# Performance work log

Measured on AMD Instinct MI355X. Metric: run time of the kernel, lower is better.

Reference implementation:

```python
import jax, jax.numpy as jnp
import numpy as np

EPS = 1e-6
K = 16
TEMP = 1.0
RES_SCALE = 0.5
CLAMP_MAX = 50.0


def _knn_indices(x, k):
    # x: (B,N,3) -> idx (B,N,k), self excluded; squared dist preserves ordering
    sq = jnp.sum(x * x, axis=-1)                      # (B,N)
    d2 = sq[:, :, None] + sq[:, None, :] - 2.0 * jnp.einsum('bnd,bmd->bnm', x, x)
    N = x.shape[1]
    eye = jnp.eye(N, dtype=bool)
    d2 = jnp.where(eye[None], jnp.inf, d2)
    _, idx = jax.lax.top_k(-d2, k)
    return idx


def _gather(t, idx):
    # t: (B,N,...), idx: (B,N,k) -> (B,N,k,...)
    return jax.vmap(lambda tb, ib: tb[ib])(t, idx)


def _vn_linear(v, W):
    return jnp.einsum('bncd,oc->bnod', v, W)


def _edge_mlp(s, W1, b1, W2, b2, W3, b3):
    h = jax.nn.silu(s @ W1.T + b1)
    h = jax.nn.silu(h @ W2.T + b2)
    return h @ W3.T + b3


def _vn_layer_norm(x, gamma, beta):
    norm = jnp.maximum(jnp.linalg.norm(x, axis=-1), EPS)      # (B,N,C)
    mean = jnp.mean(norm, axis=-1, keepdims=True)
    std = jnp.maximum(jnp.std(norm, axis=-1, keepdims=True, ddof=1), EPS)
    norm_scaled = (norm - mean) / std * gamma + beta
    return x / norm[..., None] * jnp.maximum(norm_scaled[..., None], EPS)


def _clamp_features(x, max_norm):
    n = jnp.maximum(jnp.linalg.norm(x, axis=-1, keepdims=True), EPS)
    scale = jnp.minimum(max_norm / n, 1.0)
    return x * scale


def setup_inputs() -> dict:
    key = jax.random.key(0)
    ks = jax.random.split(key, 12)
    B, N, C, Cout, H = 8, 2048, 128, 128, 32
    gain = 0.5
    lim = gain * np.sqrt(6.0 / (C + Cout))
    inp = {
        'x': jax.random.normal(ks[0], (B, N, 3), jnp.float32),
        'v': jax.random.normal(ks[1], (B, N, C, 3), jnp.float32),
        'Wq': jax.random.uniform(ks[2], (Cout, C), jnp.float32, -lim, lim),
        'Wk': jax.random.uniform(ks[3], (Cout, C), jnp.float32, -lim, lim),
        'Wu': jax.random.uniform(ks[4], (Cout, C), jnp.float32, -lim, lim),
        'W1': jax.random.normal(ks[5], (H, 4), jnp.float32) * 0.3,
        'b1': jnp.zeros((H,), jnp.float32),
        'W2': jax.random.normal(ks[6], (H, H), jnp.float32) * 0.15,
        'b2': jnp.zeros((H,), jnp.float32),
        'W3': jax.random.normal(ks[7], (1, H), jnp.float32) * 0.15,
        'b3': jnp.zeros((1,), jnp.float32),
        'gamma': jnp.ones((Cout,), jnp.float32),
        'beta': jnp.zeros((Cout,), jnp.float32),
    }
    return inp


def reference(x, v, Wq, Wk, Wu, W1, b1, W2, b2, W3, b3, gamma, beta):
    idx = _knn_indices(jax.lax.stop_gradient(x), K)           # (B,N,k)
    x_nbr = _gather(x, idx)                                    # (B,N,k,3)
    Q = _vn_linear(v, Wq)                                      # (B,N,Co,3)
    Kt = _vn_linear(v, Wk)
    U = _vn_linear(v, Wu)
    K_nbr = _gather(Kt, idx)                                   # (B,N,k,Co,3)
    U_nbr = _gather(U, idx)
    qn = jnp.mean(jnp.linalg.norm(Q, axis=-1), axis=-1, keepdims=True)   # (B,N,1)
    kn = jnp.mean(jnp.linalg.norm(Kt, axis=-1), axis=-1, keepdims=True)
    kn_nbr = _gather(kn, idx)                                  # (B,N,k,1)
    dot_nbr = jnp.mean(jnp.sum(Q[:, :, None] * K_nbr, axis=-1), axis=-1, keepdims=True)  # (B,N,k,1)
    dist = jnp.linalg.norm(x[:, :, None] - x_nbr, axis=-1, keepdims=True)                # (B,N,k,1)
    qn_exp = jnp.broadcast_to(qn[:, :, None], kn_nbr.shape)
    edge_s = jnp.concatenate([qn_exp, kn_nbr, dot_nbr, dist], axis=-1)   # (B,N,k,4)
    logits = jnp.clip(_edge_mlp(edge_s, W1, b1, W2, b2, W3, b3) / TEMP, -10.0, 10.0)
    attn = jax.nn.softmax(logits, axis=2)                      # (B,N,k,1)
    msg = jnp.sum(attn[..., None] * U_nbr, axis=2)             # (B,N,Co,3)
    out = Q + RES_SCALE * msg
    out = _vn_layer_norm(out, gamma, beta)
    out = _clamp_features(out, CLAMP_MAX)
    return out
```

## Files before the change

kernel.cpp:

```cpp
#include <hip/hip_runtime.h>
#include <math.h>

#define BB 8
#define NN 2048
#define CC 128
#define KNB 16
#define BN (BB*NN)
#define WPAD 136

#define EMPTYK 0xFFFFFFFFFFFFFFFFULL

typedef __attribute__((ext_vector_type(8))) short short8;
typedef __attribute__((ext_vector_type(4))) float floatx4;

__device__ __forceinline__ float silu_f(float x) {
  const float e = __builtin_amdgcn_exp2f(-1.442695040888963f * x);
  return x * __builtin_amdgcn_rcpf(1.0f + e);
}
__device__ __forceinline__ float fsqrt(float x) { return __builtin_amdgcn_sqrtf(x); }
__device__ __forceinline__ float frcp(float x)  { return __builtin_amdgcn_rcpf(x); }

__device__ __forceinline__ unsigned long long umin64(unsigned long long a, unsigned long long b) {
  return (b < a) ? b : a;
}

__device__ __forceinline__ unsigned short f2bf(float f) {
  unsigned u = __float_as_uint(f);
  unsigned r = u + 0x7FFFu + ((u >> 16) & 1u);
  return (unsigned short)(r >> 16);
}
__device__ __forceinline__ float bf2f(unsigned short s) {
  return __uint_as_float(((unsigned)s) << 16);
}

__device__ __forceinline__ float dot8(const float* __restrict__ w, const float* __restrict__ h) {
  const float4 a = *(const float4*)w;
  const float4 b = *(const float4*)(w + 4);
  float s = a.x*h[0];
  s = fmaf(a.y, h[1], s); s = fmaf(a.z, h[2], s); s = fmaf(a.w, h[3], s);
  s = fmaf(b.x, h[4], s); s = fmaf(b.y, h[5], s); s = fmaf(b.z, h[6], s);
  s = fmaf(b.w, h[7], s);
  return s;
}

__global__ __launch_bounds__(256) void knn_kernel(const float* __restrict__ x,
                                                  int* __restrict__ idx) {
  const int lane = threadIdx.x & 63;
  const int wave = threadIdx.x >> 6;
  const int bn = blockIdx.x * 4 + wave;
  const int b = bn >> 11;
  const int n = bn & (NN - 1);

  const float* xb = x + (size_t)b * NN * 3;
  const double xn0 = (double)xb[n*3+0], xn1 = (double)xb[n*3+1], xn2 = (double)xb[n*3+2];
  const double sqn = xn0*xn0 + xn1*xn1 + xn2*xn2;

  unsigned long long k[32];
  unsigned long long t0 = EMPTYK, t1 = EMPTYK, t2 = EMPTYK, t3 = EMPTYK;

  #pragma unroll
  for (int i = 0; i < 32; ++i) {
    const int m = i*64 + lane;
    const double a0 = (double)xb[m*3+0], a1 = (double)xb[m*3+1], a2 = (double)xb[m*3+2];
    const double sqm = a0*a0 + a1*a1 + a2*a2;
    const double dot = xn0*a0 + xn1*a1 + xn2*a2;
    const double d = sqn + sqm - 2.0*dot;
    unsigned long long kk =
        ((unsigned long long)__double_as_longlong(d) & ~2047ULL) | (unsigned long long)m;
    if (m == n) kk = 0x8000000000000000ULL | (unsigned long long)m;
    k[i] = kk;
    const bool l3 = kk < t3, l2 = kk < t2, l1 = kk < t1, l0 = kk < t0;
    t3 = l3 ? (l2 ? t2 : kk) : t3;
    t2 = l2 ? (l1 ? t1 : kk) : t2;
    t1 = l1 ? (l0 ? t0 : kk) : t1;
    t0 = l0 ? kk : t0;
  }

  int* op = idx + (size_t)bn * KNB;
  for (int t = 0; t < KNB; ++t) {
    unsigned long long g = t0;
    #pragma unroll
    for (int off = 32; off > 0; off >>= 1)
      g = umin64(g, (unsigned long long)__shfl_xor((unsigned long long)g, off, 64));

    if (lane == 0) op[t] = (int)(g & 2047ULL);

    const bool own = (t0 == g);
    t0 = own ? t1 : t0;
    t1 = own ? t2 : t1;
    t2 = own ? t3 : t2;
    t3 = own ? EMPTYK : t3;

    const bool need = (t0 == EMPTYK);
    if (__any(need)) {
      unsigned long long nm = EMPTYK;
      #pragma unroll
      for (int i = 0; i < 32; ++i) {
        const unsigned long long c = (k[i] > g) ? k[i] : EMPTYK;
        nm = umin64(nm, c);
      }
      t0 = need ? nm : t0;
    }
  }
}

__global__ __launch_bounds__(256, 2) void vn_gemm_mfma(
    const float* __restrict__ v,
    const float* __restrict__ Wq, const float* __restrict__ Wk, const float* __restrict__ Wu,
    float* __restrict__ Q, float* __restrict__ Kt, float* __restrict__ U)
{
  const int mat = blockIdx.y;
  const float* __restrict__ W = (mat == 0) ? Wq : ((mat == 1) ? Wk : Wu);
  float* __restrict__ Out = (mat == 0) ? Q : ((mat == 1) ? Kt : U);

  __shared__ short Wh[CC][WPAD];
  __shared__ short Wl[CC][WPAD];

  const int tid  = threadIdx.x;
  const int lane = tid & 63;
  const int wave = tid >> 6;
  const int quad = lane >> 4;
  const int l15  = lane & 15;

  const int m = blockIdx.x*64 + wave*16 + l15;
  const int p = m / 3, d = m - 3*p;
  const float* vb = v + (size_t)p * (CC*3) + d;
  float areg[32];
  #pragma unroll
  for (int kc = 0; kc < 4; ++kc)
    #pragma unroll
    for (int j = 0; j < 8; ++j)
      areg[kc*8+j] = vb[(kc*32 + quad*8 + j)*3];

  {
    const float4* Wg = (const float4*)W;
    #pragma unroll
    for (int it = 0; it < 16; ++it) {
      const int i = tid + it*256;
      const int o = i >> 5, c4 = (i & 31) * 4;
      float4 f = Wg[i];
      const float ff[4] = {f.x, f.y, f.z, f.w};
      short hs[4], ls[4];
      #pragma unroll
      for (int q = 0; q < 4; ++q) {
        unsigned short h = f2bf(ff[q]);
        float r = ff[q] - bf2f(h);
        hs[q] = (short)h;
        ls[q] = (short)f2bf(r);
      }
      *(short4*)&Wh[o][c4] = make_short4(hs[0], hs[1], hs[2], hs[3]);
      *(short4*)&Wl[o][c4] = make_short4(ls[0], ls[1], ls[2], ls[3]);
    }
  }

  short8 ah[4], al[4];
  #pragma unroll
  for (int kc = 0; kc < 4; ++kc)
    #pragma unroll
    for (int j = 0; j < 8; ++j) {
      const float f = areg[kc*8+j];
      unsigned short h = f2bf(f);
      float r = f - bf2f(h);
      ah[kc][j] = (short)h;
      al[kc][j] = (short)f2bf(r);
    }
  __syncthreads();

  floatx4 acc[8];
  #pragma unroll
  for (int ct = 0; ct < 8; ++ct) acc[ct] = (floatx4){0.f, 0.f, 0.f, 0.f};

  #pragma unroll
  for (int kc = 0; kc < 4; ++kc) {
    #pragma unroll
    for (int ct = 0; ct < 8; ++ct) {
      const int o = ct*16 + l15;
      const short8 bh = *(const short8*)&Wh[o][kc*32 + quad*8];
      const short8 bl = *(const short8*)&Wl[o][kc*32 + quad*8];
      acc[ct] = __builtin_amdgcn_mfma_f32_16x16x32_bf16(ah[kc], bh, acc[ct], 0, 0, 0);
      acc[ct] = __builtin_amdgcn_mfma_f32_16x16x32_bf16(al[kc], bh, acc[ct], 0, 0, 0);
      acc[ct] = __builtin_amdgcn_mfma_f32_16x16x32_bf16(ah[kc], bl, acc[ct], 0, 0, 0);
    }
  }

  const int r0 = blockIdx.x*64 + wave*16 + quad*4;
  #pragma unroll
  for (int ct = 0; ct < 8; ++ct) {
    const int o = ct*16 + l15;
    #pragma unroll
    for (int reg = 0; reg < 4; ++reg) {
      const int r = r0 + reg;
      const int pp = r / 3, dd = r - 3*pp;
      Out[(size_t)pp * (CC*3) + o*3 + dd] = acc[ct][reg];
    }
  }
}

__global__ __launch_bounds__(256) void attn_wave_kernel(
    const float* __restrict__ x, const int* __restrict__ idx,
    const float* __restrict__ Q, const float* __restrict__ Kt, const float* __restrict__ U,
    const float* __restrict__ W1, const float* __restrict__ b1,
    const float* __restrict__ W2, const float* __restrict__ b2,
    const float* __restrict__ W3, const float* __restrict__ b3,
    const float* __restrict__ gam, const float* __restrict__ bet,
    float* __restrict__ out)
{
  const int lane = threadIdx.x & 63;
  const int wv   = threadIdx.x >> 6;
  const int bn = ((blockIdx.x & 7) << 11) | (((blockIdx.x >> 3) << 2) | wv);
  const int b = bn >> 11;

  const float* Qp = Q + (size_t)bn * (CC*3) + lane*6;
  const float2 qa = *(const float2*)Qp;
  const float2 qb = *(const float2*)(Qp+2);
  const float2 qc = *(const float2*)(Qp+4);

  const int* ip = idx + (size_t)bn * KNB;
  int j[KNB];
  #pragma unroll
  for (int t = 0; t < KNB; ++t) j[t] = ip[t];

  float dpart[KNB], knp[KNB];
  #pragma unroll
  for (int t = 0; t < KNB; ++t) {
    const float* Kp = Kt + (size_t)(b*NN + j[t]) * (CC*3) + lane*6;
    const float2 a = *(const float2*)Kp;
    const float2 bb = *(const float2*)(Kp+2);
    const float2 c = *(const float2*)(Kp+4);
    dpart[t] = qa.x*a.x + qa.y*a.y + qb.x*bb.x + qb.y*bb.y + qc.x*c.x + qc.y*c.y;
    knp[t] = fsqrt(a.x*a.x + a.y*a.y + bb.x*bb.x) + fsqrt(bb.y*bb.y + c.x*c.x + c.y*c.y);
  }
  float qnp = fsqrt(qa.x*qa.x + qa.y*qa.y + qb.x*qb.x) + fsqrt(qb.y*qb.y + qc.x*qc.x + qc.y*qc.y);

  #pragma unroll
  for (int off = 1; off < 64; off <<= 1) qnp += __shfl_xor(qnp, off, 64);
  const float s0 = qnp * (1.0f/128.0f);

  float d8[8], k8[8];
  {
    const bool hb = (lane & 1) != 0;
    #pragma unroll
    for (int t = 0; t < 8; ++t) {
      const float dk = hb ? dpart[2*t+1] : dpart[2*t];
      const float dsn = hb ? dpart[2*t]  : dpart[2*t+1];
      const float kk = hb ? knp[2*t+1]   : knp[2*t];
      const float ksn = hb ? knp[2*t]    : knp[2*t+1];
      d8[t] = dk + __shfl_xor(dsn, 1, 64);
      k8[t] = kk + __shfl_xor(ksn, 1, 64);
    }
  }
  float d4[4], k4[4];
  {
    const bool hb = (lane & 2) != 0;
    #pragma unroll
    for (int t = 0; t < 4; ++t) {
      const float dk = hb ? d8[2*t+1] : d8[2*t];
      const float dsn = hb ? d8[2*t]  : d8[2*t+1];
      const float kk = hb ? k8[2*t+1] : k8[2*t];
      const float ksn = hb ? k8[2*t]  : k8[2*t+1];
      d4[t] = dk + __shfl_xor(dsn, 2, 64);
      k4[t] = kk + __shfl_xor(ksn, 2, 64);
    }
  }
  float d2a, d2b, k2a, k2b;
  {
    const bool hb = (lane & 4) != 0;
    const float dk0 = hb ? d4[1] : d4[0];
    const float dsn0 = hb ? d4[0] : d4[1];
    const float dk1 = hb ? d4[3] : d4[2];
    const float dsn1 = hb ? d4[2] : d4[3];
    d2a = dk0 + __shfl_xor(dsn0, 4, 64);
    d2b = dk1 + __shfl_xor(dsn1, 4, 64);
    const float kk0 = hb ? k4[1] : k4[0];
    const float ksn0 = hb ? k4[0] : k4[1];
    const float kk1 = hb ? k4[3] : k4[2];
    const float ksn1 = hb ? k4[2] : k4[3];
    k2a = kk0 + __shfl_xor(ksn0, 4, 64);
    k2b = kk1 + __shfl_xor(ksn1, 4, 64);
  }
  float dsel, knsel;
  {
    const bool hb = (lane & 8) != 0;
    const float dk = hb ? d2b : d2a;
    const float dsn = hb ? d2a : d2b;
    dsel = dk + __shfl_xor(dsn, 8, 64);
    const float kk = hb ? k2b : k2a;
    const float ksn = hb ? k2a : k2b;
    knsel = kk + __shfl_xor(ksn, 8, 64);
  }
  dsel  += __shfl_xor(dsel, 16, 64);
  dsel  += __shfl_xor(dsel, 32, 64);
  knsel += __shfl_xor(knsel, 16, 64);
  knsel += __shfl_xor(knsel, 32, 64);

  const int kk = lane & 15;
  int jsel = j[0];
  #pragma unroll
  for (int t = 1; t < KNB; ++t) jsel = (kk == t) ? j[t] : jsel;

  const float xi0 = x[(size_t)bn*3+0], xi1 = x[(size_t)bn*3+1], xi2 = x[(size_t)bn*3+2];
  const float* xj = x + (size_t)(b*NN + jsel)*3;
  const float dx = xi0 - xj[0], dy = xi1 - xj[1], dz = xi2 - xj[2];
  const float s3 = fsqrt(dx*dx + dy*dy + dz*dz);
  const float s1 = knsel * (1.0f/128.0f);
  const float s2 = dsel * (1.0f/128.0f);

  float u0[KNB], u1[KNB], u2[KNB], u3[KNB], u4[KNB], u5[KNB];
  #pragma unroll
  for (int t = 0; t < KNB; ++t) {
    const float* Up = U + (size_t)(b*NN + j[t]) * (CC*3) + lane*6;
    const float2 a = *(const float2*)Up;
    const float2 bb = *(const float2*)(Up+2);
    const float2 c = *(const float2*)(Up+4);
    u0[t]=a.x; u1[t]=a.y; u2[t]=bb.x; u3[t]=bb.y; u4[t]=c.x; u5[t]=c.y;
  }

  const int g = lane >> 4;
  const int o0 = g*8, o1 = (g^1)*8, o2 = (g^2)*8, o3 = (g^3)*8;

  float h1o[8];
  {
    const float4 b1a = *(const float4*)(b1 + o0);
    const float4 b1b = *(const float4*)(b1 + o0 + 4);
    const float bb1[8] = {b1a.x,b1a.y,b1a.z,b1a.w,b1b.x,b1b.y,b1b.z,b1b.w};
    #pragma unroll
    for (int jj = 0; jj < 8; ++jj) {
      const float4 w = *(const float4*)(W1 + (o0 + jj)*4);
      float u = bb1[jj];
      u = fmaf(w.x, s0, u); u = fmaf(w.y, s1, u);
      u = fmaf(w.z, s2, u); u = fmaf(w.w, s3, u);
      h1o[jj] = silu_f(u);
    }
  }
  float hx16[8], hx32[8], hx48[8];
  #pragma unroll
  for (int jj = 0; jj < 8; ++jj) hx16[jj] = __shfl_xor(h1o[jj], 16, 64);
  #pragma unroll
  for (int jj = 0; jj < 8; ++jj) hx32[jj] = __shfl_xor(h1o[jj], 32, 64);
  #pragma unroll
  for (int jj = 0; jj < 8; ++jj) hx48[jj] = __shfl_xor(hx16[jj], 32, 64);

  float logit;
  {
    const float4 b2a = *(const float4*)(b2 + o0);
    const float4 b2b = *(const float4*)(b2 + o0 + 4);
    const float bb2[8] = {b2a.x,b2a.y,b2a.z,b2a.w,b2b.x,b2b.y,b2b.z,b2b.w};
    const float4 w3a = *(const float4*)(W3 + o0);
    const float4 w3b = *(const float4*)(W3 + o0 + 4);
    const float ww3[8] = {w3a.x,w3a.y,w3a.z,w3a.w,w3b.x,w3b.y,w3b.z,w3b.w};
    float lp = 0.f;
    #pragma unroll
    for (int hh = 0; hh < 8; ++hh) {
      const float* wr = W2 + (o0 + hh)*32;
      float a = bb2[hh];
      a += dot8(wr + o0, h1o);
      a += dot8(wr + o1, hx16);
      a += dot8(wr + o2, hx32);
      a += dot8(wr + o3, hx48);
      lp = fmaf(ww3[hh], silu_f(a), lp);
    }
    lp += __shfl_xor(lp, 16, 64);
    lp += __shfl_xor(lp, 32, 64);
    logit = lp + b3[0];
  }
  logit = fminf(fmaxf(logit, -10.0f), 10.0f);

  float mx = logit;
  #pragma unroll
  for (int off = 8; off > 0; off >>= 1) mx = fmaxf(mx, __shfl_xor(mx, off, 16));
  const float e = __builtin_amdgcn_exp2f(1.442695040888963f * (logit - mx));
  float ssum = e;
  #pragma unroll
  for (int off = 8; off > 0; off >>= 1) ssum += __shfl_xor(ssum, off, 16);
  const float w = e * frcp(ssum);

  float wk[KNB];
  #pragma unroll
  for (int t = 0; t < KNB; ++t) wk[t] = __shfl(w, t, 64);

  float m0=0.f,m1=0.f,m2=0.f,m3=0.f,m4=0.f,m5=0.f;
  #pragma unroll
  for (int t = 0; t < KNB; ++t) {
    const float ww = wk[t];
    m0 = fmaf(ww, u0[t], m0); m1 = fmaf(ww, u1[t], m1); m2 = fmaf(ww, u2[t], m2);
    m3 = fmaf(ww, u3[t], m3); m4 = fmaf(ww, u4[t], m4); m5 = fmaf(ww, u5[t], m5);
  }
  const float oa0 = qa.x + 0.5f*m0, oa1 = qa.y + 0.5f*m1, oa2 = qb.x + 0.5f*m2;
  const float ob0 = qb.y + 0.5f*m3, ob1 = qc.x + 0.5f*m4, ob2 = qc.y + 0.5f*m5;

  const float na = fmaxf(fsqrt(oa0*oa0 + oa1*oa1 + oa2*oa2), 1e-6f);
  const float nb = fmaxf(fsqrt(ob0*ob0 + ob1*ob1 + ob2*ob2), 1e-6f);
  float s = na + nb;
  #pragma unroll
  for (int off = 1; off < 64; off <<= 1) s += __shfl_xor(s, off, 64);
  const float mean = s * (1.0f/128.0f);
  const float dva = na - mean, dvb = nb - mean;
  float s2v = dva*dva + dvb*dvb;
  #pragma unroll
  for (int off = 1; off < 64; off <<= 1) s2v += __shfl_xor(s2v, off, 64);
  const float stdv = fmaxf(fsqrt(s2v * (1.0f/127.0f)), 1e-6f);
  const float rstd = frcp(stdv);

  const float2 gm = *(const float2*)(gam + lane*2);
  const float2 bt = *(const float2*)(bet + lane*2);
  const float nsa = (na - mean) * rstd * gm.x + bt.x;
  const float nsb = (nb - mean) * rstd * gm.y + bt.y;
  const float sca = fmaxf(nsa, 1e-6f) * frcp(na);
  const float scb = fmaxf(nsb, 1e-6f) * frcp(nb);
  float fa0 = oa0*sca, fa1 = oa1*sca, fa2 = oa2*sca;
  float fb0 = ob0*scb, fb1 = ob1*scb, fb2 = ob2*scb;
  const float n2a = fmaxf(fsqrt(fa0*fa0 + fa1*fa1 + fa2*fa2), 1e-6f);
  const float n2b = fmaxf(fsqrt(fb0*fb0 + fb1*fb1 + fb2*fb2), 1e-6f);
  const float c2a = fminf(50.0f * frcp(n2a), 1.0f);
  const float c2b = fminf(50.0f * frcp(n2b), 1.0f);

  float* op = out + (size_t)bn * (CC*3) + lane*6;
  *(float2*)op     = make_float2(fa0*c2a, fa1*c2a);
  *(float2*)(op+2) = make_float2(fa2*c2a, fb0*c2b);
  *(float2*)(op+4) = make_float2(fb1*c2b, fb2*c2b);
}

extern "C" void kernel_launch(void* const* d_in, const int* in_sizes, int n_in,
                              void* d_out, int out_size, void* d_ws, size_t ws_size,
                              hipStream_t stream) {
  (void)in_sizes; (void)n_in; (void)out_size; (void)ws_size;
  const float* x   = (const float*)d_in[0];
  const float* v   = (const float*)d_in[1];
  const float* Wq  = (const float*)d_in[2];
  const float* Wk  = (const float*)d_in[3];
  const float* Wu  = (const float*)d_in[4];
  const float* W1  = (const float*)d_in[5];
  const float* b1  = (const float*)d_in[6];
  const float* W2  = (const float*)d_in[7];
  const float* b2  = (const float*)d_in[8];
  const float* W3  = (const float*)d_in[9];
  const float* b3  = (const float*)d_in[10];
  const float* gam = (const float*)d_in[11];
  const float* bet = (const float*)d_in[12];
  float* out = (float*)d_out;

  char* ws = (char*)d_ws;
  int*   idx = (int*)ws;
  float* Q   = (float*)(ws + (size_t)BN * KNB * 4);
  float* Kt  = Q  + (size_t)BN * CC * 3;
  float* U   = Kt + (size_t)BN * CC * 3;

  knn_kernel<<<BN/4, 256, 0, stream>>>(x, idx);
  vn_gemm_mfma<<<dim3((BN*3)/64, 3), 256, 0, stream>>>(v, Wq, Wk, Wu, Q, Kt, U);
  attn_wave_kernel<<<BN/4, 256, 0, stream>>>(x, idx, Q, Kt, U,
                                             W1, b1, W2, b2, W3, b3, gam, bet, out);
}
```

Baseline: 280.0 us.

## Precompute bf16 weight splits, reuse v tile across Q/K/U, precompute key norms

```diff
diff --git a/kernel.cpp b/kernel.cpp
--- a/kernel.cpp
+++ b/kernel.cpp
@@ -12,6 +12,7 @@
 
 typedef __attribute__((ext_vector_type(8))) short short8;
 typedef __attribute__((ext_vector_type(4))) float floatx4;
+typedef __attribute__((ext_vector_type(4), aligned(4))) float floatx4u;
 
 __device__ __forceinline__ float silu_f(float x) {
   const float e = __builtin_amdgcn_exp2f(-1.442695040888963f * x);
@@ -104,15 +105,25 @@
   }
 }
 
+__global__ __launch_bounds__(256) void wconv_kernel(
+    const float* __restrict__ Wq, const float* __restrict__ Wk, const float* __restrict__ Wu,
+    unsigned short* __restrict__ Whl)
+{
+  const int i = blockIdx.x*256 + threadIdx.x;
+  const int mat = i >> 14, rem = i & 16383;
+  const float* W = (mat == 0) ? Wq : ((mat == 1) ? Wk : Wu);
+  const float f = W[rem];
+  const unsigned short h = f2bf(f);
+  const float r = f - bf2f(h);
+  unsigned short* base = Whl + (size_t)mat * 2 * CC * CC;
+  base[rem]           = h;
+  base[CC*CC + rem]   = f2bf(r);
+}
+
 __global__ __launch_bounds__(256, 2) void vn_gemm_mfma(
-    const float* __restrict__ v,
-    const float* __restrict__ Wq, const float* __restrict__ Wk, const float* __restrict__ Wu,
+    const float* __restrict__ v, const unsigned short* __restrict__ Whl,
     float* __restrict__ Q, float* __restrict__ Kt, float* __restrict__ U)
 {
-  const int mat = blockIdx.y;
-  const float* __restrict__ W = (mat == 0) ? Wq : ((mat == 1) ? Wk : Wu);
-  float* __restrict__ Out = (mat == 0) ? Q : ((mat == 1) ? Kt : U);
-
   __shared__ short Wh[CC][WPAD];
   __shared__ short Wl[CC][WPAD];
 
@@ -131,27 +142,6 @@
     #pragma unroll
     for (int j = 0; j < 8; ++j)
       areg[kc*8+j] = vb[(kc*32 + quad*8 + j)*3];
-
-  {
-    const float4* Wg = (const float4*)W;
-    #pragma unroll
-    for (int it = 0; it < 16; ++it) {
-      const int i = tid + it*256;
-      const int o = i >> 5, c4 = (i & 31) * 4;
-      float4 f = Wg[i];
-      const float ff[4] = {f.x, f.y, f.z, f.w};
-      short hs[4], ls[4];
-      #pragma unroll
-      for (int q = 0; q < 4; ++q) {
-        unsigned short h = f2bf(ff[q]);
-        float r = ff[q] - bf2f(h);
-        hs[q] = (short)h;
-        ls[q] = (short)f2bf(r);
-      }
-      *(short4*)&Wh[o][c4] = make_short4(hs[0], hs[1], hs[2], hs[3]);
-      *(short4*)&Wl[o][c4] = make_short4(ls[0], ls[1], ls[2], ls[3]);
-    }
-  }
 
   short8 ah[4], al[4];
   #pragma unroll
@@ -164,41 +154,76 @@
       ah[kc][j] = (short)h;
       al[kc][j] = (short)f2bf(r);
     }
-  __syncthreads();
-
-  floatx4 acc[8];
-  #pragma unroll
-  for (int ct = 0; ct < 8; ++ct) acc[ct] = (floatx4){0.f, 0.f, 0.f, 0.f};
-
-  #pragma unroll
-  for (int kc = 0; kc < 4; ++kc) {
+
+  const int r0s = blockIdx.x*64 + wave*16 + quad*4;
+  int pbase[4];
+  #pragma unroll
+  for (int reg = 0; reg < 4; ++reg) {
+    const int r = r0s + reg;
+    const int pp = r / 3;
+    pbase[reg] = pp * (CC*3) + (r - 3*pp);
+  }
+  const int l153 = l15 * 3;
+
+  for (int mat = 0; mat < 3; ++mat) {
+    float* __restrict__ Out = (mat == 0) ? Q : ((mat == 1) ? Kt : U);
+    const unsigned short* Wg = Whl + (size_t)mat * 2 * CC * CC;
+
+    #pragma unroll
+    for (int it = 0; it < 8; ++it) {
+      const int i = it*256 + tid;
+      const int o = i >> 4, c8 = (i & 15) * 8;
+      *(short8*)&Wh[o][c8] = *(const short8*)&Wg[o*CC + c8];
+      *(short8*)&Wl[o][c8] = *(const short8*)&Wg[CC*CC + o*CC + c8];
+    }
+    __syncthreads();
+
+    floatx4 acc[8];
+    #pragma unroll
+    for (int ct = 0; ct < 8; ++ct) acc[ct] = (floatx4){0.f, 0.f, 0.f, 0.f};
+
+    #pragma unroll
+    for (int kc = 0; kc < 4; ++kc) {
+      #pragma unroll
+      for (int ct = 0; ct < 8; ++ct) {
+        const int o = ct*16 + l15;
+        const short8 bh = *(const short8*)&Wh[o][kc*32 + quad*8];
+        const short8 bl = *(const short8*)&Wl[o][kc*32 + quad*8];
+        acc[ct] = __builtin_amdgcn_mfma_f32_16x16x32_bf16(ah[kc], bh, acc[ct], 0, 0, 0);
+        acc[ct] = __builtin_amdgcn_mfma_f32_16x16x32_bf16(al[kc], bh, acc[ct], 0, 0, 0);
+        acc[ct] = __builtin_amdgcn_mfma_f32_16x16x32_bf16(ah[kc], bl, acc[ct], 0, 0, 0);
+      }
+    }
+    __syncthreads();
+
     #pragma unroll
     for (int ct = 0; ct < 8; ++ct) {
-      const int o = ct*16 + l15;
-      const short8 bh = *(const short8*)&Wh[o][kc*32 + quad*8];
-      const short8 bl = *(const short8*)&Wl[o][kc*32 + quad*8];
-      acc[ct] = __builtin_amdgcn_mfma_f32_16x16x32_bf16(ah[kc], bh, acc[ct], 0, 0, 0);
-      acc[ct] = __builtin_amdgcn_mfma_f32_16x16x32_bf16(al[kc], bh, acc[ct], 0, 0, 0);
-      acc[ct] = __builtin_amdgcn_mfma_f32_16x16x32_bf16(ah[kc], bl, acc[ct], 0, 0, 0);
-    }
-  }
-
-  const int r0 = blockIdx.x*64 + wave*16 + quad*4;
-  #pragma unroll
-  for (int ct = 0; ct < 8; ++ct) {
-    const int o = ct*16 + l15;
-    #pragma unroll
-    for (int reg = 0; reg < 4; ++reg) {
-      const int r = r0 + reg;
-      const int pp = r / 3, dd = r - 3*pp;
-      Out[(size_t)pp * (CC*3) + o*3 + dd] = acc[ct][reg];
-    }
-  }
+      const int o3 = ct*48 + l153;
+      #pragma unroll
+      for (int reg = 0; reg < 4; ++reg)
+        Out[pbase[reg] + o3] = acc[ct][reg];
+    }
+  }
+}
+
+__global__ __launch_bounds__(256) void kn_kernel(const float* __restrict__ Kt,
+                                                 float* __restrict__ kn) {
+  const int lane = threadIdx.x & 63;
+  const int wave = threadIdx.x >> 6;
+  const int bn = blockIdx.x * 4 + wave;
+  const float* Kp = Kt + (size_t)bn * (CC*3) + lane*6;
+  const floatx4u a = *(const floatx4u*)Kp;
+  const float2 c = *(const float2*)(Kp+4);
+  float s = fsqrt(a.x*a.x + a.y*a.y + a.z*a.z) + fsqrt(a.w*a.w + c.x*c.x + c.y*c.y);
+  #pragma unroll
+  for (int off = 1; off < 64; off <<= 1) s += __shfl_xor(s, off, 64);
+  if (lane == 0) kn[bn] = s * (1.0f/128.0f);
 }
 
 __global__ __launch_bounds__(256) void attn_wave_kernel(
     const float* __restrict__ x, const int* __restrict__ idx,
     const float* __restrict__ Q, const float* __restrict__ Kt, const float* __restrict__ U,
+    const float* __restrict__ kn,
     const float* __restrict__ W1, const float* __restrict__ b1,
     const float* __restrict__ W2, const float* __restrict__ b2,
     const float* __restrict__ W3, const float* __restrict__ b3,
@@ -211,24 +236,34 @@
   const int b = bn >> 11;
 
   const float* Qp = Q + (size_t)bn * (CC*3) + lane*6;
-  const float2 qa = *(const float2*)Qp;
-  const float2 qb = *(const float2*)(Qp+2);
-  const float2 qc = *(const float2*)(Qp+4);
+  const floatx4u q0 = *(const floatx4u*)Qp;
+  const float2 q1 = *(const float2*)(Qp+4);
+  const float2 qa = make_float2(q0.x, q0.y);
+  const float2 qb = make_float2(q0.z, q0.w);
+  const float2 qc = make_float2(q1.x, q1.y);
 
   const int* ip = idx + (size_t)bn * KNB;
   int j[KNB];
   #pragma unroll
   for (int t = 0; t < KNB; ++t) j[t] = ip[t];
 
-  float dpart[KNB], knp[KNB];
+  const int kk = lane & 15;
+  int jsel = j[0];
+  #pragma unroll
+  for (int t = 1; t < KNB; ++t) jsel = (kk == t) ? j[t] : jsel;
+
+  const float xi0 = x[(size_t)bn*3+0], xi1 = x[(size_t)bn*3+1], xi2 = x[(size_t)bn*3+2];
+  const float* xj = x + (size_t)(b*NN + jsel)*3;
+  const float xj0 = xj[0], xj1 = xj[1], xj2 = xj[2];
+  const float s1 = kn[(size_t)b*NN + jsel];
+
+  float dpart[KNB];
   #pragma unroll
   for (int t = 0; t < KNB; ++t) {
     const float* Kp = Kt + (size_t)(b*NN + j[t]) * (CC*3) + lane*6;
-    const float2 a = *(const float2*)Kp;
-    const float2 bb = *(const float2*)(Kp+2);
-    const float2 c = *(const float2*)(Kp+4);
-    dpart[t] = qa.x*a.x + qa.y*a.y + qb.x*bb.x + qb.y*bb.y + qc.x*c.x + qc.y*c.y;
-    knp[t] = fsqrt(a.x*a.x + a.y*a.y + bb.x*bb.x) + fsqrt(bb.y*bb.y + c.x*c.x + c.y*c.y);
+    const floatx4u kv = *(const floatx4u*)Kp;
+    const float2 kw = *(const float2*)(Kp+4);
+    dpart[t] = qa.x*kv.x + qa.y*kv.y + qb.x*kv.z + qb.y*kv.w + qc.x*kw.x + qc.y*kw.y;
   }
   float qnp = fsqrt(qa.x*qa.x + qa.y*qa.y + qb.x*qb.x) + fsqrt(qb.y*qb.y + qc.x*qc.x + qc.y*qc.y);
 
@@ -236,83 +271,57 @@
   for (int off = 1; off < 64; off <<= 1) qnp += __shfl_xor(qnp, off, 64);
   const float s0 = qnp * (1.0f/128.0f);
 
-  float d8[8], k8[8];
+  float d8[8];
   {
     const bool hb = (lane & 1) != 0;
     #pragma unroll
     for (int t = 0; t < 8; ++t) {
-      const float dk = hb ? dpart[2*t+1] : dpart[2*t];
-      const float dsn = hb ? dpart[2*t]  : dpart[2*t+1];
-      const float kk = hb ? knp[2*t+1]   : knp[2*t];
-      const float ksn = hb ? knp[2*t]    : knp[2*t+1];
-      d8[t] = dk + __shfl_xor(dsn, 1, 64);
-      k8[t] = kk + __shfl_xor(ksn, 1, 64);
-    }
-  }
-  float d4[4], k4[4];
+      const float keep = hb ? dpart[2*t+1] : dpart[2*t];
+      const float send = hb ? dpart[2*t]   : dpart[2*t+1];
+      d8[t] = keep + __shfl_xor(send, 1, 64);
+    }
+  }
+  float d4[4];
   {
     const bool hb = (lane & 2) != 0;
     #pragma unroll
     for (int t = 0; t < 4; ++t) {
-      const float dk = hb ? d8[2*t+1] : d8[2*t];
-      const float dsn = hb ? d8[2*t]  : d8[2*t+1];
-      const float kk = hb ? k8[2*t+1] : k8[2*t];
-      const float ksn = hb ? k8[2*t]  : k8[2*t+1];
-      d4[t] = dk + __shfl_xor(dsn, 2, 64);
-      k4[t] = kk + __shfl_xor(ksn, 2, 64);
-    }
-  }
-  float d2a, d2b, k2a, k2b;
+      const float keep = hb ? d8[2*t+1] : d8[2*t];
+      const float send = hb ? d8[2*t]   : d8[2*t+1];
+      d4[t] = keep + __shfl_xor(send, 2, 64);
+    }
+  }
+  float d2[2];
   {
     const bool hb = (lane & 4) != 0;
-    const float dk0 = hb ? d4[1] : d4[0];
-    const float dsn0 = hb ? d4[0] : d4[1];
-    const float dk1 = hb ? d4[3] : d4[2];
-    const float dsn1 = hb ? d4[2] : d4[3];
-    d2a = dk0 + __shfl_xor(dsn0, 4, 64);
-    d2b = dk1 + __shfl_xor(dsn1, 4, 64);
-    const float kk0 = hb ? k4[1] : k4[0];
-    const float ksn0 = hb ? k4[0] : k4[1];
-    const float kk1 = hb ? k4[3] : k4[2];
-    const float ksn1 = hb ? k4[2] : k4[3];
-    k2a = kk0 + __shfl_xor(ksn0, 4, 64);
-    k2b = kk1 + __shfl_xor(ksn1, 4, 64);
-  }
-  float dsel, knsel;
+    #pragma unroll
+    for (int t = 0; t < 2; ++t) {
+      const float keep = hb ? d4[2*t+1] : d4[2*t];
+      const float send = hb ? d4[2*t]   : d4[2*t+1];
+      d2[t] = keep + __shfl_xor(send, 4, 64);
+    }
+  }
+  float dsel;
   {
     const bool hb = (lane & 8) != 0;
-    const float dk = hb ? d2b : d2a;
-    const float dsn = hb ? d2a : d2b;
-    dsel = dk + __shfl_xor(dsn, 8, 64);
-    const float kk = hb ? k2b : k2a;
-    const float ksn = hb ? k2a : k2b;
-    knsel = kk + __shfl_xor(ksn, 8, 64);
-  }
-  dsel  += __shfl_xor(dsel, 16, 64);
-  dsel  += __shfl_xor(dsel, 32, 64);
-  knsel += __shfl_xor(knsel, 16, 64);
-  knsel += __shfl_xor(knsel, 32, 64);
-
-  const int kk = lane & 15;
-  int jsel = j[0];
-  #pragma unroll
-  for (int t = 1; t < KNB; ++t) jsel = (kk == t) ? j[t] : jsel;
-
-  const float xi0 = x[(size_t)bn*3+0], xi1 = x[(size_t)bn*3+1], xi2 = x[(size_t)bn*3+2];
-  const float* xj = x + (size_t)(b*NN + jsel)*3;
-  const float dx = xi0 - xj[0], dy = xi1 - xj[1], dz = xi2 - xj[2];
+    const float keep = hb ? d2[1] : d2[0];
+    const float send = hb ? d2[0] : d2[1];
+    dsel = keep + __shfl_xor(send, 8, 64);
+  }
+  dsel += __shfl_xor(dsel, 16, 64);
+  dsel += __shfl_xor(dsel, 32, 64);
+
+  const float dx = xi0 - xj0, dy = xi1 - xj1, dz = xi2 - xj2;
   const float s3 = fsqrt(dx*dx + dy*dy + dz*dz);
-  const float s1 = knsel * (1.0f/128.0f);
   const float s2 = dsel * (1.0f/128.0f);
 
   float u0[KNB], u1[KNB], u2[KNB], u3[KNB], u4[KNB], u5[KNB];
   #pragma unroll
   for (int t = 0; t < KNB; ++t) {
     const float* Up = U + (size_t)(b*NN + j[t]) * (CC*3) + lane*6;
-    const float2 a = *(const float2*)Up;
-    const float2 bb = *(const float2*)(Up+2);
-    const float2 c = *(const float2*)(Up+4);
-    u0[t]=a.x; u1[t]=a.y; u2[t]=bb.x; u3[t]=bb.y; u4[t]=c.x; u5[t]=c.y;
+    const floatx4u uv = *(const floatx4u*)Up;
+    const float2 uw = *(const float2*)(Up+4);
+    u0[t]=uv.x; u1[t]=uv.y; u2[t]=uv.z; u3[t]=uv.w; u4[t]=uw.x; u5[t]=uw.y;
   }
 
   const int g = lane >> 4;
@@ -415,8 +424,8 @@
   const float c2b = fminf(50.0f * frcp(n2b), 1.0f);
 
   float* op = out + (size_t)bn * (CC*3) + lane*6;
-  *(float2*)op     = make_float2(fa0*c2a, fa1*c2a);
-  *(float2*)(op+2) = make_float2(fa2*c2a, fb0*c2b);
+  floatx4u o4; o4.x = fa0*c2a; o4.y = fa1*c2a; o4.z = fa2*c2a; o4.w = fb0*c2b;
+  *(floatx4u*)op = o4;
   *(float2*)(op+4) = make_float2(fb1*c2b, fb2*c2b);
 }
 
@@ -444,9 +453,13 @@
   float* Q   = (float*)(ws + (size_t)BN * KNB * 4);
   float* Kt  = Q  + (size_t)BN * CC * 3;
   float* U   = Kt + (size_t)BN * CC * 3;
+  unsigned short* Whl = (unsigned short*)(U + (size_t)BN * CC * 3);
+  float* kn  = (float*)((char*)Whl + (size_t)3 * 2 * CC * CC * 2);
 
   knn_kernel<<<BN/4, 256, 0, stream>>>(x, idx);
-  vn_gemm_mfma<<<dim3((BN*3)/64, 3), 256, 0, stream>>>(v, Wq, Wk, Wu, Q, Kt, U);
-  attn_wave_kernel<<<BN/4, 256, 0, stream>>>(x, idx, Q, Kt, U,
+  wconv_kernel<<<192, 256, 0, stream>>>(Wq, Wk, Wu, Whl);
+  vn_gemm_mfma<<<(BN*3)/64, 256, 0, stream>>>(v, Whl, Q, Kt, U);
+  kn_kernel<<<BN/4, 256, 0, stream>>>(Kt, kn);
+  attn_wave_kernel<<<BN/4, 256, 0, stream>>>(x, idx, Q, Kt, U, kn,
                                              W1, b1, W2, b2, W3, b3, gam, bet, out);
 }
```

Result: no change. 279.3 us (-0.3%).
